# Kernel tuning notes

Hardware: AMD Instinct MI355X
Metric: run time of the kernel (lower is better)

The kernel has to match this reference:

```python
import jax, jax.numpy as jnp
import numpy as np

N = 2048          # n_nodes
H = 8             # nheads
ALPHA = 0.2       # leaky-relu slope
NEG = -9e15       # mask value used by pyGAT
# (in_dim, per-head hidden, out_dim) for the six GAT blocks of GMHAAE(256, ...)
DIMS = [(256, 128, 128), (128, 256, 256), (256, 512, 384),
        (384, 512, 256), (256, 256, 128), (128, 128, 256)]


def setup_inputs() -> dict:
    key = jax.random.key(0)
    ks = jax.random.split(key, 64)
    inp = {}
    inp["x"] = jax.random.normal(ks[0], (N, 256), dtype=jnp.float32)
    a = (jax.random.uniform(ks[1], (N, N)) < 0.01).astype(jnp.float32)
    adj = jnp.clip(jnp.maximum(a, a.T) + jnp.eye(N, dtype=jnp.float32), 0.0, 1.0)
    inp["adj"] = adj
    ki = 2
    for i, (fin, hid, fout) in enumerate(DIMS, start=1):
        s1 = (2.0 / (fin + hid)) ** 0.5
        inp[f"p{i}_Wh"] = jax.random.normal(ks[ki], (H, fin, hid), dtype=jnp.float32) * s1; ki += 1
        inp[f"p{i}_ah"] = jax.random.normal(ks[ki], (H, 2 * hid), dtype=jnp.float32) * 0.1; ki += 1
        s2 = (2.0 / (H * hid + fout)) ** 0.5
        inp[f"p{i}_Wo"] = jax.random.normal(ks[ki], (H * hid, fout), dtype=jnp.float32) * s2; ki += 1
        inp[f"p{i}_ao"] = jax.random.normal(ks[ki], (2 * fout,), dtype=jnp.float32) * 0.1; ki += 1
    return inp


def _gat_block(x, adj, Wh, ah, Wo, ao):
    """pyGAT GAT block: H concat heads (elu) -> single out head -> elu. Eval mode (no dropout)."""
    n = x.shape[0]
    D = Wh.shape[2]
    h = jnp.einsum('nf,hfd->hnd', x, Wh)                       # [H,N,D]
    s1 = jnp.einsum('hnd,hd->hn', h, ah[:, :D])                # a^T [Wh_i]
    s2 = jnp.einsum('hnd,hd->hn', h, ah[:, D:])                # a^T [Wh_j]
    e = jax.nn.leaky_relu(s1[:, :, None] + s2[:, None, :], ALPHA)   # [H,N,N]
    att = jax.nn.softmax(jnp.where(adj[None] > 0, e, NEG), axis=-1)
    hcat = jax.nn.elu(jnp.einsum('hnm,hmd->hnd', att, h))      # concat=True -> elu per head
    hcat = hcat.transpose(1, 0, 2).reshape(n, -1)              # [N, H*D]
    # output attention head (concat=False)
    D2 = Wo.shape[1]
    ho = hcat @ Wo                                             # [N,D2]
    eo = jax.nn.leaky_relu((ho @ ao[:D2])[:, None] + (ho @ ao[D2:])[None, :], ALPHA)
    ato = jax.nn.softmax(jnp.where(adj > 0, eo, NEG), axis=-1)
    return jax.nn.elu(ato @ ho)                                # F.elu in GAT.forward


def reference(x, adj,
              p1_Wh, p1_ah, p1_Wo, p1_ao,
              p2_Wh, p2_ah, p2_Wo, p2_ao,
              p3_Wh, p3_ah, p3_Wo, p3_ao,
              p4_Wh, p4_ah, p4_Wo, p4_ao,
              p5_Wh, p5_ah, p5_Wo, p5_ao,
              p6_Wh, p6_ah, p6_Wo, p6_ao):
    layers = [(p1_Wh, p1_ah, p1_Wo, p1_ao), (p2_Wh, p2_ah, p2_Wo, p2_ao),
              (p3_Wh, p3_ah, p3_Wo, p3_ao), (p4_Wh, p4_ah, p4_Wo, p4_ao),
              (p5_Wh, p5_ah, p5_Wo, p5_ao), (p6_Wh, p6_ah, p6_Wo, p6_ao)]
    h = x
    for (Wh, ah, Wo, ao) in layers:   # fixed 6-layer encoder-decoder stack
        h = _gat_block(h, adj, Wh, ah, Wo, ao)
    return h
```

## Files before the change

kernel.cpp:

```cpp
#include <hip/hip_runtime.h>
#include <hip/hip_bf16.h>
#include <math.h>

#define NN 2048
#define NH 8
#define LRALPHA 0.2f

typedef short bf16x8 __attribute__((ext_vector_type(8)));
typedef float f32x4  __attribute__((ext_vector_type(4)));

static __device__ __forceinline__ float lrelu(float x){ return x > 0.f ? x : LRALPHA * x; }
static __device__ __forceinline__ float elu(float x){ return x > 0.f ? x : expm1f(x); }

static __device__ __forceinline__ unsigned short f2bf(float v){
    unsigned u = __float_as_uint(v);
    unsigned r = (u + 0x7fffu + ((u >> 16) & 1u)) >> 16;
    return (unsigned short)r;
}
static __device__ __forceinline__ float bf2f(unsigned short b){
    return __uint_as_float(((unsigned)b) << 16);
}
static __device__ __forceinline__ float blo(unsigned u){ return __uint_as_float(u << 16); }
static __device__ __forceinline__ float bhi(unsigned u){ return __uint_as_float(u & 0xffff0000u); }

static __device__ __forceinline__ void gload16(const void* g, void* l){
    __builtin_amdgcn_global_load_lds((const __attribute__((address_space(1))) void*)g,
                                     (__attribute__((address_space(3))) void*)l, 16, 0, 0);
}

__global__ void k_count(const float* __restrict__ adj, int* __restrict__ deg) {
    int gw   = (blockIdx.x * blockDim.x + threadIdx.x) >> 6;
    int lane = threadIdx.x & 63;
    if (gw >= NN) return;
    const float* row = adj + (size_t)gw * NN;
    int cnt = 0;
    for (int j = lane; j < NN; j += 64) cnt += (row[j] > 0.f) ? 1 : 0;
    #pragma unroll
    for (int off = 32; off; off >>= 1) cnt += __shfl_down(cnt, off);
    if (lane == 0) deg[gw] = cnt;
}

__global__ void k_scan(const int* __restrict__ deg, int* __restrict__ rp) {
    __shared__ int a[NN], b[NN];
    int t = threadIdx.x;
    for (int i = t; i < NN; i += 1024) a[i] = deg[i];
    __syncthreads();
    int* src = a; int* dst = b;
    for (int off = 1; off < NN; off <<= 1) {
        for (int i = t; i < NN; i += 1024)
            dst[i] = src[i] + (i >= off ? src[i - off] : 0);
        __syncthreads();
        int* tmp = src; src = dst; dst = tmp;
    }
    for (int i = t; i < NN; i += 1024) rp[i + 1] = src[i];
    if (t == 0) rp[0] = 0;
}

__global__ void k_fill(const float* __restrict__ adj, const int* __restrict__ rp,
                       int* __restrict__ ci) {
    int gw   = (blockIdx.x * blockDim.x + threadIdx.x) >> 6;
    int lane = threadIdx.x & 63;
    if (gw >= NN) return;
    const float* row = adj + (size_t)gw * NN;
    int base = rp[gw];
    for (int j0 = 0; j0 < NN; j0 += 64) {
        bool v = row[j0 + lane] > 0.f;
        unsigned long long m = __ballot(v);
        int pos = __popcll(m & ((1ULL << lane) - 1ULL));
        if (v) ci[base + pos] = j0 + lane;
        base += __popcll(m);
    }
}

__global__ void k_split(const float* __restrict__ src, unsigned short* __restrict__ hi,
                        unsigned short* __restrict__ lo, int n4) {
    int i = blockIdx.x * 256 + threadIdx.x;
    if (i >= n4) return;
    float4 v = ((const float4*)src)[i];
    ushort4 h, l;
    h.x = f2bf(v.x); l.x = f2bf(v.x - bf2f(h.x));
    h.y = f2bf(v.y); l.y = f2bf(v.y - bf2f(h.y));
    h.z = f2bf(v.z); l.z = f2bf(v.z - bf2f(h.z));
    h.w = f2bf(v.w); l.w = f2bf(v.w - bf2f(h.w));
    ((ushort4*)hi)[i] = h;
    ((ushort4*)lo)[i] = l;
}

struct TSDesc {
    const float* B[12];
    unsigned short* bh[12];
    unsigned short* bl[12];
    int K[12], Nc[12], hs[12];
    int start[13];
};

__global__ __launch_bounds__(256) void k_tsplit_all(TSDesc d) {
    __shared__ float t[64][65];
    int b = blockIdx.x;
    int s = 0;
    while (b >= d.start[s + 1]) s++;
    int lb = b - d.start[s];
    int K = d.K[s], Nc = d.Nc[s], hs = d.hs[s];
    int tilesX = K >> 6;
    int kb = (lb % tilesX) * 64, cb = (lb / tilesX) * 64;
    const float* B = d.B[s];
    unsigned short* bth = d.bh[s];
    unsigned short* btl = d.bl[s];

    int tid = threadIdx.x;
    #pragma unroll
    for (int i = 0; i < 16; i++) {
        int idx = i * 256 + tid;
        int kk = idx >> 6, cc = idx & 63;
        int c = cb + cc, k = kb + kk;
        float v;
        if (hs < 0) v = B[(size_t)k * Nc + c];
        else {
            int hid = 1 << hs; int head = c >> hs; int dd = c & (hid - 1);
            v = B[((size_t)head * K + k) * hid + dd];
        }
        t[kk][cc] = v;
    }
    __syncthreads();
    #pragma unroll
    for (int i = 0; i < 16; i++) {
        int idx = i * 256 + tid;
        int cc = idx >> 6, kk = idx & 63;
        float v = t[kk][cc];
        unsigned short h = f2bf(v);
        size_t o = (size_t)(cb + cc) * K + kb + kk;
        bth[o] = h;
        btl[o] = f2bf(v - bf2f(h));
    }
}

template<int OUT, int NT>
__global__ __launch_bounds__(256) void k_mfma(
    const unsigned short* __restrict__ Ah, const unsigned short* __restrict__ Al,
    const unsigned short* __restrict__ Bh, const unsigned short* __restrict__ Bl,
    float* __restrict__ Cf, unsigned short* __restrict__ Cb, int Nc, int K, int Kc,
    const float* __restrict__ avec, float* __restrict__ sg1, float* __restrict__ sg2,
    int hs, int aoff, int nx, int nz, int zcol)
{
    constexpr int ALB = 4096;
    constexpr int BHB = (NT == 3) ? 8192 : 4096;
    constexpr int BLB = BHB + 2048;
    __shared__ unsigned short lds[(NT == 3) ? 12288 : 8192];
    int tid = threadIdx.x, lane = tid & 63, w = tid >> 6;

    int g = blockIdx.x;
    int xcd = g & 7, q = g >> 3;
    int x, y, z;
    if (zcol) {
        int zper = nz >> 3;
        z = xcd + 8 * (q % zper);
        int r = q / zper;
        int nxy = nx * 16;
        int r2 = r + xcd * (nxy >> 3); if (r2 >= nxy) r2 -= nxy;
        x = r2 % nx; y = r2 / nx;
    } else {
        y = xcd + 8 * (q & 1);
        x = q >> 1; z = 0;
    }
    int m0 = y * 128, n0 = x * 64;
    int kbeg = z * Kc;

    int ra0 = tid >> 2;       int ga0 = ((tid & 3) - (ra0 >> 1)) & 3;
    int ra1 = 64 + (tid >> 2); int ga1 = ((tid & 3) - (ra1 >> 1)) & 3;
    int rb  = tid >> 2;       int gb  = ((tid & 3) - (rb >> 1)) & 3;
    const unsigned short* pAh0 = Ah + (size_t)(m0 + ra0) * K + kbeg + ga0 * 8;
    const unsigned short* pAh1 = Ah + (size_t)(m0 + ra1) * K + kbeg + ga1 * 8;
    const unsigned short* pAl0 = (NT == 3) ? Al + (size_t)(m0 + ra0) * K + kbeg + ga0 * 8 : nullptr;
    const unsigned short* pAl1 = (NT == 3) ? Al + (size_t)(m0 + ra1) * K + kbeg + ga1 * 8 : nullptr;
    const unsigned short* pBh  = Bh + (size_t)(n0 + rb) * K + kbeg + gb * 8;
    const unsigned short* pBl  = Bl + (size_t)(n0 + rb) * K + kbeg + gb * 8;
    unsigned short* dA0 = &lds[w * 512];
    unsigned short* dA1 = &lds[2048 + w * 512];
    unsigned short* dB  = &lds[BHB + w * 512];

    int wr = w >> 1, wc = w & 1;
    int offA[4], offB[2];
    #pragma unroll
    for (int m = 0; m < 4; m++) {
        int row = wr * 64 + m * 16 + (lane & 15); int gg = lane >> 4;
        offA[m] = (row * 4 + ((gg + (row >> 1)) & 3)) * 8;
    }
    #pragma unroll
    for (int n = 0; n < 2; n++) {
        int row = wc * 32 + n * 16 + (lane & 15); int gg = lane >> 4;
        offB[n] = (row * 4 + ((gg + (row >> 1)) & 3)) * 8;
    }

    f32x4 acc[4][2];
    #pragma unroll
    for (int m = 0; m < 4; m++)
        #pragma unroll
        for (int n = 0; n < 2; n++) acc[m][n] = (f32x4){0.f, 0.f, 0.f, 0.f};

    int nk = Kc >> 5;
    for (int ks = 0; ks < nk; ks++) {
        gload16(pAh0, dA0);
        gload16(pAh1, dA1);
        if (NT == 3) { gload16(pAl0, dA0 + ALB); gload16(pAl1, dA1 + ALB); }
        gload16(pBh, dB);
        gload16(pBl, dB + 2048);
        pAh0 += 32; pAh1 += 32;
        if (NT == 3) { pAl0 += 32; pAl1 += 32; }
        pBh += 32; pBl += 32;
        __syncthreads();
        bf16x8 ah[4], al[4], bh[2], bl[2];
        #pragma unroll
        for (int m = 0; m < 4; m++) {
            ah[m] = *(const bf16x8*)&lds[offA[m]];
            if (NT == 3) al[m] = *(const bf16x8*)&lds[ALB + offA[m]];
        }
        #pragma unroll
        for (int n = 0; n < 2; n++) {
            bh[n] = *(const bf16x8*)&lds[BHB + offB[n]];
            bl[n] = *(const bf16x8*)&lds[BLB + offB[n]];
        }
        #pragma unroll
        for (int m = 0; m < 4; m++)
            #pragma unroll
            for (int n = 0; n < 2; n++) {
                acc[m][n] = __builtin_amdgcn_mfma_f32_16x16x32_bf16(ah[m], bh[n], acc[m][n], 0, 0, 0);
                if (NT == 3)
                    acc[m][n] = __builtin_amdgcn_mfma_f32_16x16x32_bf16(al[m], bh[n], acc[m][n], 0, 0, 0);
                acc[m][n] = __builtin_amdgcn_mfma_f32_16x16x32_bf16(ah[m], bl[n], acc[m][n], 0, 0, 0);
            }
        __syncthreads();
    }

    size_t pbase = (size_t)z * NN * Nc;
    #pragma unroll
    for (int m = 0; m < 4; m++)
        #pragma unroll
        for (int n = 0; n < 2; n++) {
            int row = m0 + wr * 64 + m * 16 + (lane >> 4) * 4;
            int col = n0 + wc * 32 + n * 16 + (lane & 15);
            #pragma unroll
            for (int r = 0; r < 4; r++) {
                float v = acc[m][n][r];
                if (OUT == 0) Cb[(size_t)(row + r) * Nc + col] = f2bf(v);
                else          Cf[pbase + (size_t)(row + r) * Nc + col] = v;
            }
        }

    if (OUT == 0) {
        int head = (hs >= 0) ? (n0 >> hs) : 0;
        const float* ab = avec + head * 2 * aoff;
        float av1[2], av2[2];
        int colbase = n0 + wc * 32 + (lane & 15);
        #pragma unroll
        for (int n = 0; n < 2; n++) {
            int c = colbase + n * 16;
            int dd = (hs >= 0) ? (c & (aoff - 1)) : c;
            av1[n] = ab[dd];
            av2[n] = ab[dd + aoff];
        }
        #pragma unroll
        for (int m = 0; m < 4; m++)
            #pragma unroll
            for (int r = 0; r < 4; r++) {
                float p1 = 0.f, p2 = 0.f;
                #pragma unroll
                for (int n = 0; n < 2; n++) {
                    float v = acc[m][n][r];
                    p1 += v * av1[n];
                    p2 += v * av2[n];
                }
                #pragma unroll
                for (int o = 1; o < 16; o <<= 1) {
                    p1 += __shfl_xor(p1, o);
                    p2 += __shfl_xor(p2, o);
                }
                if ((lane & 15) == 0) {
                    int row = m0 + wr * 64 + m * 16 + (lane >> 4) * 4 + r;
                    atomicAdd(&sg1[head * NN + row], p1);
                    atomicAdd(&sg2[head * NN + row], p2);
                }
            }
    }
}

__global__ __launch_bounds__(256) void k_red(
    const float* __restrict__ part, float* __restrict__ ho,
    const float* __restrict__ ao, float* __restrict__ t1, float* __restrict__ t2,
    int fout, int sko)
{
    int wid = threadIdx.x >> 6;
    int lane = threadIdx.x & 63;
    int row = blockIdx.x * 4 + wid;
    int C4 = fout >> 2;
    const float4* p4 = (const float4*)part;
    size_t stride4 = (size_t)NN * C4;
    float d1 = 0.f, d2 = 0.f;
    for (int c = lane; c < C4; c += 64) {
        size_t o = (size_t)row * C4 + c;
        float4 s = p4[o];
        for (int zz = 1; zz < sko; zz++) {
            float4 v = p4[o + (size_t)zz * stride4];
            s.x += v.x; s.y += v.y; s.z += v.z; s.w += v.w;
        }
        ((float4*)ho)[o] = s;
        int cc = c * 4;
        d1 += s.x * ao[cc]        + s.y * ao[cc + 1]
            + s.z * ao[cc + 2]    + s.w * ao[cc + 3];
        d2 += s.x * ao[fout + cc]     + s.y * ao[fout + cc + 1]
            + s.z * ao[fout + cc + 2] + s.w * ao[fout + cc + 3];
    }
    #pragma unroll
    for (int o = 32; o; o >>= 1) { d1 += __shfl_xor(d1, o); d2 += __shfl_xor(d2, o); }
    if (lane == 0) { t1[row] = d1; t2[row] = d2; }
}

__global__ __launch_bounds__(256) void k_aggb(
    const unsigned short* __restrict__ hh, const float* __restrict__ s1,
    const float* __restrict__ s2, const int* __restrict__ rp, const int* __restrict__ ci,
    unsigned short* __restrict__ outH, int hid, int HD, int c8sh)
{
    __shared__ float    wls[256];
    __shared__ unsigned cls[256];

    int tid = threadIdx.x;
    int wid = tid >> 6;
    int lane = tid & 63;
    int head = blockIdx.x & (NH - 1);
    int i    = (blockIdx.x >> 3) * 4 + wid;
    float* wlsw = wls + wid * 64;
    unsigned* clsw = cls + wid * 64;

    int base = rp[i], deg = rp[i + 1] - base;
    float s1i = s1[head * NN + i];
    const float* s2h = s2 + head * NN;

    int C8  = 1 << c8sh;
    int G   = 64 >> c8sh;
    int col = lane & (C8 - 1);
    int grp = lane >> c8sh;

    const uint4* h4 = (const uint4*)hh;
    unsigned hoff8 = (unsigned)(head * hid) >> 3;
    unsigned ld8   = (unsigned)HD >> 3;

    float m_run = -1e30f, s_run = 0.f;
    float a0=0,a1=0,a2=0,a3=0,a4=0,a5=0,a6=0,a7=0;

    for (int k0 = 0; k0 < deg; k0 += 64) {
        int n = min(64, deg - k0);
        float e = -1e30f;
        unsigned coff = 0;
        if (lane < n) {
            int j = ci[base + k0 + lane];
            e = lrelu(s1i + s2h[j]);
            coff = (unsigned)j * ld8 + hoff8;
        }
        float bm = e;
        #pragma unroll
        for (int o = 32; o; o >>= 1) bm = fmaxf(bm, __shfl_xor(bm, o));
        float m2 = fmaxf(m_run, bm);
        float wv = (lane < n) ? expf(e - m2) : 0.f;
        float bs = wv;
        #pragma unroll
        for (int o = 32; o; o >>= 1) bs += __shfl_xor(bs, o);
        float scale = expf(m_run - m2);
        s_run = s_run * scale + bs;
        a0*=scale; a1*=scale; a2*=scale; a3*=scale;
        a4*=scale; a5*=scale; a6*=scale; a7*=scale;
        m_run = m2;
        wlsw[lane] = wv;
        clsw[lane] = coff;

        float q0=0,q1=0,q2=0,q3=0,q4=0,q5=0,q6=0,q7=0;
        int k = grp;
        for (; k + G < n; k += 2 * G) {
            float w0 = wlsw[k], w1 = wlsw[k + G];
            uint4 u0 = h4[clsw[k]     + col];
            uint4 u1 = h4[clsw[k + G] + col];
            a0 += w0 * blo(u0.x); a1 += w0 * bhi(u0.x);
            a2 += w0 * blo(u0.y); a3 += w0 * bhi(u0.y);
            a4 += w0 * blo(u0.z); a5 += w0 * bhi(u0.z);
            a6 += w0 * blo(u0.w); a7 += w0 * bhi(u0.w);
            q0 += w1 * blo(u1.x); q1 += w1 * bhi(u1.x);
            q2 += w1 * blo(u1.y); q3 += w1 * bhi(u1.y);
            q4 += w1 * blo(u1.z); q5 += w1 * bhi(u1.z);
            q6 += w1 * blo(u1.w); q7 += w1 * bhi(u1.w);
        }
        if (k < n) {
            float w0 = wlsw[k];
            uint4 u0 = h4[clsw[k] + col];
            a0 += w0 * blo(u0.x); a1 += w0 * bhi(u0.x);
            a2 += w0 * blo(u0.y); a3 += w0 * bhi(u0.y);
            a4 += w0 * blo(u0.z); a5 += w0 * bhi(u0.z);
            a6 += w0 * blo(u0.w); a7 += w0 * bhi(u0.w);
        }
        a0+=q0; a1+=q1; a2+=q2; a3+=q3; a4+=q4; a5+=q5; a6+=q6; a7+=q7;
    }

    #pragma unroll
    for (int o = 64; o > 1; o >>= 1) {
        if (o > C8) {
            int m = o >> 1;
            a0 += __shfl_xor(a0, m); a1 += __shfl_xor(a1, m);
            a2 += __shfl_xor(a2, m); a3 += __shfl_xor(a3, m);
            a4 += __shfl_xor(a4, m); a5 += __shfl_xor(a5, m);
            a6 += __shfl_xor(a6, m); a7 += __shfl_xor(a7, m);
        }
    }

    if (grp == 0) {
        float inv = 1.f / s_run;
        float v[8] = {a0*inv,a1*inv,a2*inv,a3*inv,a4*inv,a5*inv,a6*inv,a7*inv};
        #pragma unroll
        for (int e2 = 0; e2 < 8; e2++) v[e2] = elu(v[e2]);
        unsigned short hh_[8];
        #pragma unroll
        for (int e2 = 0; e2 < 8; e2++) hh_[e2] = f2bf(v[e2]);
        size_t ob = ((size_t)i * HD + head * hid) >> 3;
        uint4 ph;
        ph.x = (unsigned)hh_[0] | ((unsigned)hh_[1] << 16);
        ph.y = (unsigned)hh_[2] | ((unsigned)hh_[3] << 16);
        ph.z = (unsigned)hh_[4] | ((unsigned)hh_[5] << 16);
        ph.w = (unsigned)hh_[6] | ((unsigned)hh_[7] << 16);
        ((uint4*)outH)[ob + col] = ph;
    }
}

__global__ __launch_bounds__(256) void k_aggs(
    const float* __restrict__ hsrc, const float* __restrict__ t1, const float* __restrict__ t2,
    const int* __restrict__ rp, const int* __restrict__ ci,
    float* __restrict__ outF, unsigned short* __restrict__ outH,
    int fout, int SCtot)
{
    __shared__ float    wls[256];
    __shared__ unsigned cls[256];

    int tid = threadIdx.x;
    int wid = tid >> 6;
    int lane = tid & 63;
    int task = blockIdx.x * 4 + wid;
    int i   = task / SCtot;
    int sc  = task - i * SCtot;
    float* wlsw = wls + wid * 64;
    unsigned* clsw = cls + wid * 64;

    int base = rp[i], deg = rp[i + 1] - base;
    float s1i = t1[i];

    int C4tot = fout >> 2;
    int soff  = sc * 64;
    int C4s   = min(64, C4tot - soff);
    int c4sh  = 31 - __clz(C4s);
    int col = lane & (C4s - 1);
    int grp = lane >> c4sh;
    int G   = 64 >> c4sh;

    const float4* h4 = (const float4*)hsrc;
    unsigned ld4 = (unsigned)fout >> 2;

    float m_run = -1e30f, s_run = 0.f;
    float4 acc = make_float4(0.f, 0.f, 0.f, 0.f);

    for (int k0 = 0; k0 < deg; k0 += 64) {
        int n = min(64, deg - k0);
        float e = -1e30f;
        unsigned coff = 0;
        if (lane < n) {
            int j = ci[base + k0 + lane];
            e = lrelu(s1i + t2[j]);
            coff = (unsigned)j * ld4 + soff;
        }
        float bm = e;
        #pragma unroll
        for (int o = 32; o; o >>= 1) bm = fmaxf(bm, __shfl_xor(bm, o));
        float m2 = fmaxf(m_run, bm);
        float wv = (lane < n) ? expf(e - m2) : 0.f;
        float bs = wv;
        #pragma unroll
        for (int o = 32; o; o >>= 1) bs += __shfl_xor(bs, o);
        float scale = expf(m_run - m2);
        s_run = s_run * scale + bs;
        acc.x *= scale; acc.y *= scale; acc.z *= scale; acc.w *= scale;
        m_run = m2;
        wlsw[lane] = wv;
        clsw[lane] = coff;

        float4 q = make_float4(0,0,0,0);
        int k = grp;
        for (; k + G < n; k += 2 * G) {
            float w0 = wlsw[k], w1 = wlsw[k + G];
            float4 h0 = h4[clsw[k]     + col];
            float4 h1 = h4[clsw[k + G] + col];
            acc.x += w0 * h0.x; acc.y += w0 * h0.y; acc.z += w0 * h0.z; acc.w += w0 * h0.w;
            q.x   += w1 * h1.x; q.y   += w1 * h1.y; q.z   += w1 * h1.z; q.w   += w1 * h1.w;
        }
        if (k < n) {
            float w0 = wlsw[k];
            float4 h0 = h4[clsw[k] + col];
            acc.x += w0 * h0.x; acc.y += w0 * h0.y; acc.z += w0 * h0.z; acc.w += w0 * h0.w;
        }
        acc.x += q.x; acc.y += q.y; acc.z += q.z; acc.w += q.w;
    }

    #pragma unroll
    for (int o = 64; o > 1; o >>= 1) {
        if (o > C4s) {
            int m = o >> 1;
            acc.x += __shfl_xor(acc.x, m); acc.y += __shfl_xor(acc.y, m);
            acc.z += __shfl_xor(acc.z, m); acc.w += __shfl_xor(acc.w, m);
        }
    }

    if (grp == 0) {
        float inv = 1.f / s_run;
        float4 val;
        val.x = elu(acc.x * inv); val.y = elu(acc.y * inv);
        val.z = elu(acc.z * inv); val.w = elu(acc.w * inv);
        size_t o4 = (size_t)i * ld4 + soff + col;
        if (outF) ((float4*)outF)[o4] = val;
        ushort4 h;
        h.x = f2bf(val.x); h.y = f2bf(val.y);
        h.z = f2bf(val.z); h.w = f2bf(val.w);
        ((ushort4*)outH)[o4] = h;
    }
}

extern "C" void kernel_launch(void* const* d_in, const int* in_sizes, int n_in,
                              void* d_out, int out_size, void* d_ws, size_t ws_size,
                              hipStream_t stream)
{
    const float* x   = (const float*)d_in[0];
    const float* adj = (const float*)d_in[1];
    struct L { int fin, hid, fout; };
    const L dims[6] = {{256,128,128},{128,256,256},{256,512,384},
                       {384,512,256},{256,256,128},{128,128,256}};
    const int SKwo[6] = {16, 8, 8, 8, 16, 8};
    const int SB = 2 * NH * NN;

    char* ws = (char*)d_ws;
    size_t off = 0;
    auto alloc = [&](size_t bytes) -> void* {
        void* p = ws + off;
        off = (off + bytes + 255) & ~(size_t)255;
        return p;
    };
    int*   rp   = (int*)alloc((NN + 1) * sizeof(int));
    int*   deg  = (int*)alloc(NN * sizeof(int));
    int*   ci   = (int*)alloc((size_t)(1 << 20) * sizeof(int));
    unsigned short* hh  = (unsigned short*)alloc((size_t)NN * 4096 * 2);
    unsigned short* ghi = (unsigned short*)alloc((size_t)NN * 4096 * 2);
    unsigned short* xhi = (unsigned short*)alloc((size_t)NN * 512 * 2);
    unsigned short* xlo = (unsigned short*)alloc((size_t)NN * 512 * 2);
    float* sball  = (float*)alloc((size_t)6 * SB * sizeof(float));
    float* hopart = (float*)alloc((size_t)NN * 3072 * sizeof(float));
    float* ho     = (float*)alloc((size_t)NN * 384 * sizeof(float));
    float* t12    = (float*)alloc((size_t)2 * NN * sizeof(float));

    unsigned short* whh[6]; unsigned short* whl[6];
    unsigned short* woh[6]; unsigned short* wol[6];
    TSDesc td;
    int nblk = 0;
    for (int l = 0; l < 6; l++) {
        int fin = dims[l].fin, hid = dims[l].hid, fout = dims[l].fout;
        int HD = NH * hid;
        size_t szWh = (size_t)fin * HD, szWo = (size_t)HD * fout;
        whh[l] = (unsigned short*)alloc(szWh * 2);
        whl[l] = (unsigned short*)alloc(szWh * 2);
        woh[l] = (unsigned short*)alloc(szWo * 2);
        wol[l] = (unsigned short*)alloc(szWo * 2);
        int hs = (hid == 128) ? 7 : (hid == 256) ? 8 : 9;
        td.B[2*l] = (const float*)d_in[2 + l * 4 + 0];
        td.bh[2*l] = whh[l]; td.bl[2*l] = whl[l];
        td.K[2*l] = fin; td.Nc[2*l] = HD; td.hs[2*l] = hs;
        td.start[2*l] = nblk; nblk += (fin / 64) * (HD / 64);
        td.B[2*l+1] = (const float*)d_in[2 + l * 4 + 2];
        td.bh[2*l+1] = woh[l]; td.bl[2*l+1] = wol[l];
        td.K[2*l+1] = HD; td.Nc[2*l+1] = fout; td.hs[2*l+1] = -1;
        td.start[2*l+1] = nblk; nblk += (HD / 64) * (fout / 64);
    }
    td.start[12] = nblk;

    hipMemsetAsync(sball, 0, (size_t)6 * SB * sizeof(float), stream);
    k_count<<<NN / 4, 256, 0, stream>>>(adj, deg);
    k_scan <<<1, 1024, 0, stream>>>(deg, rp);
    k_fill <<<NN / 4, 256, 0, stream>>>(adj, rp, ci);
    k_split<<<(NN * 256 / 4 + 255) / 256, 256, 0, stream>>>(x, xhi, xlo, NN * 256 / 4);
    k_tsplit_all<<<nblk, 256, 0, stream>>>(td);

    for (int l = 0; l < 6; l++) {
        int fin = dims[l].fin, hid = dims[l].hid, fout = dims[l].fout;
        int HD = NH * hid;
        int hs = (hid == 128) ? 7 : (hid == 256) ? 8 : 9;
        int c8sh = hs - 3;
        const float* ah = (const float*)d_in[2 + l * 4 + 1];
        const float* ao = (const float*)d_in[2 + l * 4 + 3];

        float* s1 = sball + (size_t)l * SB;
        float* s2 = s1 + NH * NN;
        float* t1 = t12;
        float* t2 = t12 + NN;

        int nx1 = HD / 64;
        if (l == 0)
            k_mfma<0,3><<<nx1 * 16, 256, 0, stream>>>(xhi, xlo, whh[l], whl[l], nullptr, hh, HD,
                                                      fin, fin, ah, s1, s2, hs, hid, nx1, 1, 0);
        else
            k_mfma<0,2><<<nx1 * 16, 256, 0, stream>>>(xhi, nullptr, whh[l], whl[l], nullptr, hh, HD,
                                                      fin, fin, ah, s1, s2, hs, hid, nx1, 1, 0);

        k_aggb<<<NN * NH / 4, 256, 0, stream>>>(hh, s1, s2, rp, ci, ghi, hid, HD, c8sh);

        int sko = SKwo[l];
        int nx2 = fout / 64;
        k_mfma<1,2><<<nx2 * 16 * sko, 256, 0, stream>>>(ghi, nullptr, woh[l], wol[l], hopart,
                                                        nullptr, fout, HD, HD / sko,
                                                        nullptr, nullptr, nullptr, -1, fout,
                                                        nx2, sko, 1);

        k_red<<<NN / 4, 256, 0, stream>>>(hopart, ho, ao, t1, t2, fout, sko);

        float* outF = (l == 5) ? (float*)d_out : nullptr;
        int SCtot = (fout / 4 + 63) / 64;
        k_aggs<<<NN * SCtot / 4, 256, 0, stream>>>(ho, t1, t2, rp, ci, outF, xhi, fout, SCtot);
    }
}
```

Measured before the change: 454.8 us.

## Precompute normalized edge softmax weights in separate kernels before aggregation

Splits each attention aggregation into two kernels. A new kernel computes normalized softmax weights per edge (per head) with a two-pass max/sum over the CSR neighbors and stores them in a workspace buffer. The aggregation kernels then just load these weights and drop the online-softmax rescaling and the final normalization. This avoids recomputing the softmax in every column-slice/head block, at the cost of extra kernel launches, an extra pass over the neighbor lists, and weight-buffer traffic. EMAX caps the edge count at 131072.

```diff
diff --git a/kernel.cpp b/kernel.cpp
--- a/kernel.cpp
+++ b/kernel.cpp
@@ -5,6 +5,7 @@
 #define NN 2048
 #define NH 8
 #define LRALPHA 0.2f
+#define EMAX (1 << 17)
 
 typedef short bf16x8 __attribute__((ext_vector_type(8)));
 typedef float f32x4  __attribute__((ext_vector_type(4)));
@@ -314,9 +315,83 @@
     if (lane == 0) { t1[row] = d1; t2[row] = d2; }
 }
 
-__global__ __launch_bounds__(256) void k_aggb(
-    const unsigned short* __restrict__ hh, const float* __restrict__ s1,
-    const float* __restrict__ s2, const int* __restrict__ rp, const int* __restrict__ ci,
+__global__ __launch_bounds__(256) void k_w(
+    const float* __restrict__ s1, const float* __restrict__ s2,
+    const int* __restrict__ rp, const int* __restrict__ ci,
+    float* __restrict__ wt)
+{
+    int wid = threadIdx.x >> 6, lane = threadIdx.x & 63;
+    int i = blockIdx.x * 4 + wid;
+    int base = rp[i], deg = rp[i + 1] - base;
+    #pragma unroll 1
+    for (int h = 0; h < NH; h++) {
+        float s1i = s1[h * NN + i];
+        const float* s2h = s2 + h * NN;
+        float m = -1e30f, s = 0.f;
+        for (int k0 = 0; k0 < deg; k0 += 64) {
+            int n = min(64, deg - k0);
+            float e = -1e30f;
+            if (lane < n) e = lrelu(s1i + s2h[ci[base + k0 + lane]]);
+            float bm = e;
+            #pragma unroll
+            for (int o = 32; o; o >>= 1) bm = fmaxf(bm, __shfl_xor(bm, o));
+            float m2 = fmaxf(m, bm);
+            float wv = (lane < n) ? expf(e - m2) : 0.f;
+            float bs = wv;
+            #pragma unroll
+            for (int o = 32; o; o >>= 1) bs += __shfl_xor(bs, o);
+            s = s * expf(m - m2) + bs;
+            m = m2;
+        }
+        float inv = 1.f / s;
+        for (int k0 = 0; k0 < deg; k0 += 64) {
+            int n = min(64, deg - k0);
+            if (lane < n) {
+                float e = lrelu(s1i + s2h[ci[base + k0 + lane]]);
+                wt[(size_t)h * EMAX + base + k0 + lane] = expf(e - m) * inv;
+            }
+        }
+    }
+}
+
+__global__ __launch_bounds__(256) void k_wo(
+    const float* __restrict__ t1, const float* __restrict__ t2,
+    const int* __restrict__ rp, const int* __restrict__ ci,
+    float* __restrict__ wto)
+{
+    int wid = threadIdx.x >> 6, lane = threadIdx.x & 63;
+    int i = blockIdx.x * 4 + wid;
+    int base = rp[i], deg = rp[i + 1] - base;
+    float s1i = t1[i];
+    float m = -1e30f, s = 0.f;
+    for (int k0 = 0; k0 < deg; k0 += 64) {
+        int n = min(64, deg - k0);
+        float e = -1e30f;
+        if (lane < n) e = lrelu(s1i + t2[ci[base + k0 + lane]]);
+        float bm = e;
+        #pragma unroll
+        for (int o = 32; o; o >>= 1) bm = fmaxf(bm, __shfl_xor(bm, o));
+        float m2 = fmaxf(m, bm);
+        float wv = (lane < n) ? expf(e - m2) : 0.f;
+        float bs = wv;
+        #pragma unroll
+        for (int o = 32; o; o >>= 1) bs += __shfl_xor(bs, o);
+        s = s * expf(m - m2) + bs;
+        m = m2;
+    }
+    float inv = 1.f / s;
+    for (int k0 = 0; k0 < deg; k0 += 64) {
+        int n = min(64, deg - k0);
+        if (lane < n) {
+            float e = lrelu(s1i + t2[ci[base + k0 + lane]]);
+            wto[base + k0 + lane] = expf(e - m) * inv;
+        }
+    }
+}
+
+__global__ __launch_bounds__(256) void k_gab(
+    const unsigned short* __restrict__ hh, const float* __restrict__ wt,
+    const int* __restrict__ rp, const int* __restrict__ ci,
     unsigned short* __restrict__ outH, int hid, int HD, int c8sh)
 {
     __shared__ float    wls[256];
@@ -331,8 +406,7 @@
     unsigned* clsw = cls + wid * 64;
 
     int base = rp[i], deg = rp[i + 1] - base;
-    float s1i = s1[head * NN + i];
-    const float* s2h = s2 + head * NN;
+    const float* wth = wt + (size_t)head * EMAX + base;
 
     int C8  = 1 << c8sh;
     int G   = 64 >> c8sh;
@@ -343,34 +417,14 @@
     unsigned hoff8 = (unsigned)(head * hid) >> 3;
     unsigned ld8   = (unsigned)HD >> 3;
 
-    float m_run = -1e30f, s_run = 0.f;
     float a0=0,a1=0,a2=0,a3=0,a4=0,a5=0,a6=0,a7=0;
 
     for (int k0 = 0; k0 < deg; k0 += 64) {
         int n = min(64, deg - k0);
-        float e = -1e30f;
-        unsigned coff = 0;
         if (lane < n) {
-            int j = ci[base + k0 + lane];
-            e = lrelu(s1i + s2h[j]);
-            coff = (unsigned)j * ld8 + hoff8;
-        }
-        float bm = e;
-        #pragma unroll
-        for (int o = 32; o; o >>= 1) bm = fmaxf(bm, __shfl_xor(bm, o));
-        float m2 = fmaxf(m_run, bm);
-        float wv = (lane < n) ? expf(e - m2) : 0.f;
-        float bs = wv;
-        #pragma unroll
-        for (int o = 32; o; o >>= 1) bs += __shfl_xor(bs, o);
-        float scale = expf(m_run - m2);
-        s_run = s_run * scale + bs;
-        a0*=scale; a1*=scale; a2*=scale; a3*=scale;
-        a4*=scale; a5*=scale; a6*=scale; a7*=scale;
-        m_run = m2;
-        wlsw[lane] = wv;
-        clsw[lane] = coff;
-
+            wlsw[lane] = wth[k0 + lane];
+            clsw[lane] = (unsigned)ci[base + k0 + lane] * ld8 + hoff8;
+        }
         float q0=0,q1=0,q2=0,q3=0,q4=0,q5=0,q6=0,q7=0;
         int k = grp;
         for (; k + G < n; k += 2 * G) {
@@ -409,8 +463,7 @@
     }
 
     if (grp == 0) {
-        float inv = 1.f / s_run;
-        float v[8] = {a0*inv,a1*inv,a2*inv,a3*inv,a4*inv,a5*inv,a6*inv,a7*inv};
+        float v[8] = {a0,a1,a2,a3,a4,a5,a6,a7};
         #pragma unroll
         for (int e2 = 0; e2 < 8; e2++) v[e2] = elu(v[e2]);
         unsigned short hh_[8];
@@ -426,8 +479,8 @@
     }
 }
 
-__global__ __launch_bounds__(256) void k_aggs(
-    const float* __restrict__ hsrc, const float* __restrict__ t1, const float* __restrict__ t2,
+__global__ __launch_bounds__(256) void k_gas(
+    const float* __restrict__ hsrc, const float* __restrict__ wto,
     const int* __restrict__ rp, const int* __restrict__ ci,
     float* __restrict__ outF, unsigned short* __restrict__ outH,
     int fout, int SCtot)
@@ -445,7 +498,6 @@
     unsigned* clsw = cls + wid * 64;
 
     int base = rp[i], deg = rp[i + 1] - base;
-    float s1i = t1[i];
 
     int C4tot = fout >> 2;
     int soff  = sc * 64;
@@ -458,33 +510,14 @@
     const float4* h4 = (const float4*)hsrc;
     unsigned ld4 = (unsigned)fout >> 2;
 
-    float m_run = -1e30f, s_run = 0.f;
     float4 acc = make_float4(0.f, 0.f, 0.f, 0.f);
 
     for (int k0 = 0; k0 < deg; k0 += 64) {
         int n = min(64, deg - k0);
-        float e = -1e30f;
-        unsigned coff = 0;
         if (lane < n) {
-            int j = ci[base + k0 + lane];
-            e = lrelu(s1i + t2[j]);
-            coff = (unsigned)j * ld4 + soff;
-        }
-        float bm = e;
-        #pragma unroll
-        for (int o = 32; o; o >>= 1) bm = fmaxf(bm, __shfl_xor(bm, o));
-        float m2 = fmaxf(m_run, bm);
-        float wv = (lane < n) ? expf(e - m2) : 0.f;
-        float bs = wv;
-        #pragma unroll
-        for (int o = 32; o; o >>= 1) bs += __shfl_xor(bs, o);
-        float scale = expf(m_run - m2);
-        s_run = s_run * scale + bs;
-        acc.x *= scale; acc.y *= scale; acc.z *= scale; acc.w *= scale;
-        m_run = m2;
-        wlsw[lane] = wv;
-        clsw[lane] = coff;
-
+            wlsw[lane] = wto[base + k0 + lane];
+            clsw[lane] = (unsigned)ci[base + k0 + lane] * ld4 + soff;
+        }
         float4 q = make_float4(0,0,0,0);
         int k = grp;
         for (; k + G < n; k += 2 * G) {
@@ -512,10 +545,9 @@
     }
 
     if (grp == 0) {
-        float inv = 1.f / s_run;
         float4 val;
-        val.x = elu(acc.x * inv); val.y = elu(acc.y * inv);
-        val.z = elu(acc.z * inv); val.w = elu(acc.w * inv);
+        val.x = elu(acc.x); val.y = elu(acc.y);
+        val.z = elu(acc.z); val.w = elu(acc.w);
         size_t o4 = (size_t)i * ld4 + soff + col;
         if (outF) ((float4*)outF)[o4] = val;
         ushort4 h;
@@ -555,6 +587,8 @@
     float* hopart = (float*)alloc((size_t)NN * 3072 * sizeof(float));
     float* ho     = (float*)alloc((size_t)NN * 384 * sizeof(float));
     float* t12    = (float*)alloc((size_t)2 * NN * sizeof(float));
+    float* wt     = (float*)alloc((size_t)NH * EMAX * sizeof(float));
+    float* wto    = (float*)alloc((size_t)EMAX * sizeof(float));
 
     unsigned short* whh[6]; unsigned short* whl[6];
     unsigned short* woh[6]; unsigned short* wol[6];
@@ -608,7 +642,8 @@
             k_mfma<0,2><<<nx1 * 16, 256, 0, stream>>>(xhi, nullptr, whh[l], whl[l], nullptr, hh, HD,
                                                       fin, fin, ah, s1, s2, hs, hid, nx1, 1, 0);
 
-        k_aggb<<<NN * NH / 4, 256, 0, stream>>>(hh, s1, s2, rp, ci, ghi, hid, HD, c8sh);
+        k_w<<<NN / 4, 256, 0, stream>>>(s1, s2, rp, ci, wt);
+        k_gab<<<NN * NH / 4, 256, 0, stream>>>(hh, wt, rp, ci, ghi, hid, HD, c8sh);
 
         int sko = SKwo[l];
         int nx2 = fout / 64;
@@ -619,8 +654,9 @@
 
         k_red<<<NN / 4, 256, 0, stream>>>(hopart, ho, ao, t1, t2, fout, sko);
 
+        k_wo<<<NN / 4, 256, 0, stream>>>(t1, t2, rp, ci, wto);
         float* outF = (l == 5) ? (float*)d_out : nullptr;
         int SCtot = (fout / 4 + 63) / 64;
-        k_aggs<<<NN * SCtot / 4, 256, 0, stream>>>(ho, t1, t2, rp, ci, outF, xhi, fout, SCtot);
-    }
-}
+        k_gas<<<NN * SCtot / 4, 256, 0, stream>>>(ho, wto, rp, ci, outF, xhi, fout, SCtot);
+    }
+}
```

New measurement: 561.7 us. +23.5%, slower.

## Store split-K output partials and ho in bf16, rework output aggregation

Applied to the files above, without the earlier changes.

The split-K output GEMM now writes bf16 partials instead of fp32. The reduction kernel sums these into a bf16 ho buffer, and the output-head aggregation gathers 8 bf16 values per lane with one wave per node instead of column-sliced float4 tasks. Split-K is also fixed at 8 for all layers. This halves the bytes moved for the partials and ho gathers, at the cost of extra rounding error from bf16 partial sums and bf16 ho, and idle lanes when fout is 384.

```diff
diff --git a/kernel.cpp b/kernel.cpp
--- a/kernel.cpp
+++ b/kernel.cpp
@@ -27,6 +27,12 @@
     __builtin_amdgcn_global_load_lds((const __attribute__((address_space(1))) void*)g,
                                      (__attribute__((address_space(3))) void*)l, 16, 0, 0);
 }
+
+#define ACC8(A, wv, u) \
+    A[0] += wv * blo(u.x); A[1] += wv * bhi(u.x); \
+    A[2] += wv * blo(u.y); A[3] += wv * bhi(u.y); \
+    A[4] += wv * blo(u.z); A[5] += wv * bhi(u.z); \
+    A[6] += wv * blo(u.w); A[7] += wv * bhi(u.w);
 
 __global__ void k_count(const float* __restrict__ adj, int* __restrict__ deg) {
     int gw   = (blockIdx.x * blockDim.x + threadIdx.x) >> 6;
@@ -138,7 +144,7 @@
 __global__ __launch_bounds__(256) void k_mfma(
     const unsigned short* __restrict__ Ah, const unsigned short* __restrict__ Al,
     const unsigned short* __restrict__ Bh, const unsigned short* __restrict__ Bl,
-    float* __restrict__ Cf, unsigned short* __restrict__ Cb, int Nc, int K, int Kc,
+    unsigned short* __restrict__ Cb, int Nc, int K, int Kc,
     const float* __restrict__ avec, float* __restrict__ sg1, float* __restrict__ sg2,
     int hs, int aoff, int nx, int nz, int zcol)
 {
@@ -239,11 +245,8 @@
             int row = m0 + wr * 64 + m * 16 + (lane >> 4) * 4;
             int col = n0 + wc * 32 + n * 16 + (lane & 15);
             #pragma unroll
-            for (int r = 0; r < 4; r++) {
-                float v = acc[m][n][r];
-                if (OUT == 0) Cb[(size_t)(row + r) * Nc + col] = f2bf(v);
-                else          Cf[pbase + (size_t)(row + r) * Nc + col] = v;
-            }
+            for (int r = 0; r < 4; r++)
+                Cb[pbase + (size_t)(row + r) * Nc + col] = f2bf(acc[m][n][r]);
         }
 
     if (OUT == 0) {
@@ -284,30 +287,41 @@
 }
 
 __global__ __launch_bounds__(256) void k_red(
-    const float* __restrict__ part, float* __restrict__ ho,
+    const unsigned short* __restrict__ part, unsigned short* __restrict__ ho,
     const float* __restrict__ ao, float* __restrict__ t1, float* __restrict__ t2,
     int fout, int sko)
 {
     int wid = threadIdx.x >> 6;
     int lane = threadIdx.x & 63;
     int row = blockIdx.x * 4 + wid;
-    int C4 = fout >> 2;
-    const float4* p4 = (const float4*)part;
-    size_t stride4 = (size_t)NN * C4;
+    int C8 = fout >> 3;
+    const uint4* p8 = (const uint4*)part;
+    size_t stride8 = (size_t)NN * C8;
     float d1 = 0.f, d2 = 0.f;
-    for (int c = lane; c < C4; c += 64) {
-        size_t o = (size_t)row * C4 + c;
-        float4 s = p4[o];
-        for (int zz = 1; zz < sko; zz++) {
-            float4 v = p4[o + (size_t)zz * stride4];
-            s.x += v.x; s.y += v.y; s.z += v.z; s.w += v.w;
-        }
-        ((float4*)ho)[o] = s;
-        int cc = c * 4;
-        d1 += s.x * ao[cc]        + s.y * ao[cc + 1]
-            + s.z * ao[cc + 2]    + s.w * ao[cc + 3];
-        d2 += s.x * ao[fout + cc]     + s.y * ao[fout + cc + 1]
-            + s.z * ao[fout + cc + 2] + s.w * ao[fout + cc + 3];
+    if (lane < C8) {
+        size_t o = (size_t)row * C8 + lane;
+        float s[8];
+        #pragma unroll
+        for (int e = 0; e < 8; e++) s[e] = 0.f;
+        for (int zz = 0; zz < sko; zz++) {
+            uint4 u = p8[o + (size_t)zz * stride8];
+            ACC8(s, 1.f, u);
+        }
+        unsigned short hb[8];
+        #pragma unroll
+        for (int e = 0; e < 8; e++) hb[e] = f2bf(s[e]);
+        uint4 ph;
+        ph.x = (unsigned)hb[0] | ((unsigned)hb[1] << 16);
+        ph.y = (unsigned)hb[2] | ((unsigned)hb[3] << 16);
+        ph.z = (unsigned)hb[4] | ((unsigned)hb[5] << 16);
+        ph.w = (unsigned)hb[6] | ((unsigned)hb[7] << 16);
+        ((uint4*)ho)[o] = ph;
+        int cc = lane * 8;
+        #pragma unroll
+        for (int e = 0; e < 8; e++) {
+            d1 += s[e] * ao[cc + e];
+            d2 += s[e] * ao[fout + cc + e];
+        }
     }
     #pragma unroll
     for (int o = 32; o; o >>= 1) { d1 += __shfl_xor(d1, o); d2 += __shfl_xor(d2, o); }
@@ -344,7 +358,9 @@
     unsigned ld8   = (unsigned)HD >> 3;
 
     float m_run = -1e30f, s_run = 0.f;
-    float a0=0,a1=0,a2=0,a3=0,a4=0,a5=0,a6=0,a7=0;
+    float aA[8], qB[8];
+    #pragma unroll
+    for (int e = 0; e < 8; e++) { aA[e] = 0.f; qB[e] = 0.f; }
 
     for (int k0 = 0; k0 < deg; k0 += 64) {
         int n = min(64, deg - k0);
@@ -365,72 +381,56 @@
         for (int o = 32; o; o >>= 1) bs += __shfl_xor(bs, o);
         float scale = expf(m_run - m2);
         s_run = s_run * scale + bs;
-        a0*=scale; a1*=scale; a2*=scale; a3*=scale;
-        a4*=scale; a5*=scale; a6*=scale; a7*=scale;
+        #pragma unroll
+        for (int e2 = 0; e2 < 8; e2++) aA[e2] *= scale;
         m_run = m2;
         wlsw[lane] = wv;
         clsw[lane] = coff;
 
-        float q0=0,q1=0,q2=0,q3=0,q4=0,q5=0,q6=0,q7=0;
         int k = grp;
         for (; k + G < n; k += 2 * G) {
             float w0 = wlsw[k], w1 = wlsw[k + G];
             uint4 u0 = h4[clsw[k]     + col];
             uint4 u1 = h4[clsw[k + G] + col];
-            a0 += w0 * blo(u0.x); a1 += w0 * bhi(u0.x);
-            a2 += w0 * blo(u0.y); a3 += w0 * bhi(u0.y);
-            a4 += w0 * blo(u0.z); a5 += w0 * bhi(u0.z);
-            a6 += w0 * blo(u0.w); a7 += w0 * bhi(u0.w);
-            q0 += w1 * blo(u1.x); q1 += w1 * bhi(u1.x);
-            q2 += w1 * blo(u1.y); q3 += w1 * bhi(u1.y);
-            q4 += w1 * blo(u1.z); q5 += w1 * bhi(u1.z);
-            q6 += w1 * blo(u1.w); q7 += w1 * bhi(u1.w);
+            ACC8(aA, w0, u0);
+            ACC8(qB, w1, u1);
         }
         if (k < n) {
             float w0 = wlsw[k];
             uint4 u0 = h4[clsw[k] + col];
-            a0 += w0 * blo(u0.x); a1 += w0 * bhi(u0.x);
-            a2 += w0 * blo(u0.y); a3 += w0 * bhi(u0.y);
-            a4 += w0 * blo(u0.z); a5 += w0 * bhi(u0.z);
-            a6 += w0 * blo(u0.w); a7 += w0 * bhi(u0.w);
-        }
-        a0+=q0; a1+=q1; a2+=q2; a3+=q3; a4+=q4; a5+=q5; a6+=q6; a7+=q7;
-    }
-
-    #pragma unroll
-    for (int o = 64; o > 1; o >>= 1) {
-        if (o > C8) {
-            int m = o >> 1;
-            a0 += __shfl_xor(a0, m); a1 += __shfl_xor(a1, m);
-            a2 += __shfl_xor(a2, m); a3 += __shfl_xor(a3, m);
-            a4 += __shfl_xor(a4, m); a5 += __shfl_xor(a5, m);
-            a6 += __shfl_xor(a6, m); a7 += __shfl_xor(a7, m);
+            ACC8(aA, w0, u0);
+        }
+    }
+    #pragma unroll
+    for (int e2 = 0; e2 < 8; e2++) aA[e2] += qB[e2];
+
+    #pragma unroll
+    for (int m = 32; m >= 1; m >>= 1) {
+        if (m >= C8) {
+            #pragma unroll
+            for (int e2 = 0; e2 < 8; e2++) aA[e2] += __shfl_xor(aA[e2], m);
         }
     }
 
     if (grp == 0) {
         float inv = 1.f / s_run;
-        float v[8] = {a0*inv,a1*inv,a2*inv,a3*inv,a4*inv,a5*inv,a6*inv,a7*inv};
-        #pragma unroll
-        for (int e2 = 0; e2 < 8; e2++) v[e2] = elu(v[e2]);
-        unsigned short hh_[8];
-        #pragma unroll
-        for (int e2 = 0; e2 < 8; e2++) hh_[e2] = f2bf(v[e2]);
+        unsigned short hb[8];
+        #pragma unroll
+        for (int e2 = 0; e2 < 8; e2++) hb[e2] = f2bf(elu(aA[e2] * inv));
         size_t ob = ((size_t)i * HD + head * hid) >> 3;
         uint4 ph;
-        ph.x = (unsigned)hh_[0] | ((unsigned)hh_[1] << 16);
-        ph.y = (unsigned)hh_[2] | ((unsigned)hh_[3] << 16);
-        ph.z = (unsigned)hh_[4] | ((unsigned)hh_[5] << 16);
-        ph.w = (unsigned)hh_[6] | ((unsigned)hh_[7] << 16);
+        ph.x = (unsigned)hb[0] | ((unsigned)hb[1] << 16);
+        ph.y = (unsigned)hb[2] | ((unsigned)hb[3] << 16);
+        ph.z = (unsigned)hb[4] | ((unsigned)hb[5] << 16);
+        ph.w = (unsigned)hb[6] | ((unsigned)hb[7] << 16);
         ((uint4*)outH)[ob + col] = ph;
     }
 }
 
 __global__ __launch_bounds__(256) void k_aggs(
-    const float* __restrict__ hsrc, const float* __restrict__ t1, const float* __restrict__ t2,
-    const int* __restrict__ rp, const int* __restrict__ ci,
-    float* __restrict__ outF, unsigned short* __restrict__ outH,
-    int fout, int SCtot)
+    const unsigned short* __restrict__ ho, const float* __restrict__ t1,
+    const float* __restrict__ t2, const int* __restrict__ rp, const int* __restrict__ ci,
+    float* __restrict__ outF, unsigned short* __restrict__ outH, int fout)
 {
     __shared__ float    wls[256];
     __shared__ unsigned cls[256];
@@ -438,28 +438,28 @@
     int tid = threadIdx.x;
     int wid = tid >> 6;
     int lane = tid & 63;
-    int task = blockIdx.x * 4 + wid;
-    int i   = task / SCtot;
-    int sc  = task - i * SCtot;
+    int i = blockIdx.x * 4 + wid;
     float* wlsw = wls + wid * 64;
     unsigned* clsw = cls + wid * 64;
 
     int base = rp[i], deg = rp[i + 1] - base;
     float s1i = t1[i];
 
-    int C4tot = fout >> 2;
-    int soff  = sc * 64;
-    int C4s   = min(64, C4tot - soff);
-    int c4sh  = 31 - __clz(C4s);
-    int col = lane & (C4s - 1);
-    int grp = lane >> c4sh;
-    int G   = 64 >> c4sh;
-
-    const float4* h4 = (const float4*)hsrc;
-    unsigned ld4 = (unsigned)fout >> 2;
+    int C8s = fout >> 3;
+    int G, col, grp; bool act;
+    if (C8s == 48) { G = 1; col = lane; grp = 0; act = lane < 48; }
+    else {
+        int sh = 31 - __clz(C8s);
+        G = 64 >> sh; col = lane & (C8s - 1); grp = lane >> sh; act = true;
+    }
+
+    const uint4* h4 = (const uint4*)ho;
+    unsigned ld8 = (unsigned)fout >> 3;
 
     float m_run = -1e30f, s_run = 0.f;
-    float4 acc = make_float4(0.f, 0.f, 0.f, 0.f);
+    float aA[8], qB[8];
+    #pragma unroll
+    for (int e = 0; e < 8; e++) { aA[e] = 0.f; qB[e] = 0.f; }
 
     for (int k0 = 0; k0 < deg; k0 += 64) {
         int n = min(64, deg - k0);
@@ -468,7 +468,7 @@
         if (lane < n) {
             int j = ci[base + k0 + lane];
             e = lrelu(s1i + t2[j]);
-            coff = (unsigned)j * ld4 + soff;
+            coff = (unsigned)j * ld8;
         }
         float bm = e;
         #pragma unroll
@@ -480,48 +480,59 @@
         for (int o = 32; o; o >>= 1) bs += __shfl_xor(bs, o);
         float scale = expf(m_run - m2);
         s_run = s_run * scale + bs;
-        acc.x *= scale; acc.y *= scale; acc.z *= scale; acc.w *= scale;
+        #pragma unroll
+        for (int e2 = 0; e2 < 8; e2++) aA[e2] *= scale;
         m_run = m2;
         wlsw[lane] = wv;
         clsw[lane] = coff;
 
-        float4 q = make_float4(0,0,0,0);
-        int k = grp;
-        for (; k + G < n; k += 2 * G) {
-            float w0 = wlsw[k], w1 = wlsw[k + G];
-            float4 h0 = h4[clsw[k]     + col];
-            float4 h1 = h4[clsw[k + G] + col];
-            acc.x += w0 * h0.x; acc.y += w0 * h0.y; acc.z += w0 * h0.z; acc.w += w0 * h0.w;
-            q.x   += w1 * h1.x; q.y   += w1 * h1.y; q.z   += w1 * h1.z; q.w   += w1 * h1.w;
-        }
-        if (k < n) {
-            float w0 = wlsw[k];
-            float4 h0 = h4[clsw[k] + col];
-            acc.x += w0 * h0.x; acc.y += w0 * h0.y; acc.z += w0 * h0.z; acc.w += w0 * h0.w;
-        }
-        acc.x += q.x; acc.y += q.y; acc.z += q.z; acc.w += q.w;
-    }
-
-    #pragma unroll
-    for (int o = 64; o > 1; o >>= 1) {
-        if (o > C4s) {
-            int m = o >> 1;
-            acc.x += __shfl_xor(acc.x, m); acc.y += __shfl_xor(acc.y, m);
-            acc.z += __shfl_xor(acc.z, m); acc.w += __shfl_xor(acc.w, m);
-        }
-    }
-
-    if (grp == 0) {
+        if (act) {
+            int k = grp;
+            for (; k + G < n; k += 2 * G) {
+                float w0 = wlsw[k], w1 = wlsw[k + G];
+                uint4 u0 = h4[clsw[k]     + col];
+                uint4 u1 = h4[clsw[k + G] + col];
+                ACC8(aA, w0, u0);
+                ACC8(qB, w1, u1);
+            }
+            if (k < n) {
+                float w0 = wlsw[k];
+                uint4 u0 = h4[clsw[k] + col];
+                ACC8(aA, w0, u0);
+            }
+        }
+    }
+    #pragma unroll
+    for (int e2 = 0; e2 < 8; e2++) aA[e2] += qB[e2];
+
+    #pragma unroll
+    for (int m = 32; m >= 1; m >>= 1) {
+        if (m >= C8s) {
+            #pragma unroll
+            for (int e2 = 0; e2 < 8; e2++) aA[e2] += __shfl_xor(aA[e2], m);
+        }
+    }
+
+    if (grp == 0 && act) {
         float inv = 1.f / s_run;
-        float4 val;
-        val.x = elu(acc.x * inv); val.y = elu(acc.y * inv);
-        val.z = elu(acc.z * inv); val.w = elu(acc.w * inv);
-        size_t o4 = (size_t)i * ld4 + soff + col;
-        if (outF) ((float4*)outF)[o4] = val;
-        ushort4 h;
-        h.x = f2bf(val.x); h.y = f2bf(val.y);
-        h.z = f2bf(val.z); h.w = f2bf(val.w);
-        ((ushort4*)outH)[o4] = h;
+        float v[8];
+        #pragma unroll
+        for (int e2 = 0; e2 < 8; e2++) v[e2] = elu(aA[e2] * inv);
+        size_t ob = (size_t)i * C8s + col;
+        if (outF) {
+            size_t o4 = ob * 2;
+            ((float4*)outF)[o4]     = make_float4(v[0], v[1], v[2], v[3]);
+            ((float4*)outF)[o4 + 1] = make_float4(v[4], v[5], v[6], v[7]);
+        }
+        unsigned short hb[8];
+        #pragma unroll
+        for (int e2 = 0; e2 < 8; e2++) hb[e2] = f2bf(v[e2]);
+        uint4 ph;
+        ph.x = (unsigned)hb[0] | ((unsigned)hb[1] << 16);
+        ph.y = (unsigned)hb[2] | ((unsigned)hb[3] << 16);
+        ph.z = (unsigned)hb[4] | ((unsigned)hb[5] << 16);
+        ph.w = (unsigned)hb[6] | ((unsigned)hb[7] << 16);
+        ((uint4*)outH)[ob] = ph;
     }
 }
 
@@ -534,7 +545,7 @@
     struct L { int fin, hid, fout; };
     const L dims[6] = {{256,128,128},{128,256,256},{256,512,384},
                        {384,512,256},{256,256,128},{128,128,256}};
-    const int SKwo[6] = {16, 8, 8, 8, 16, 8};
+    const int SKO = 8;
     const int SB = 2 * NH * NN;
 
     char* ws = (char*)d_ws;
@@ -552,8 +563,8 @@
     unsigned short* xhi = (unsigned short*)alloc((size_t)NN * 512 * 2);
     unsigned short* xlo = (unsigned short*)alloc((size_t)NN * 512 * 2);
     float* sball  = (float*)alloc((size_t)6 * SB * sizeof(float));
-    float* hopart = (float*)alloc((size_t)NN * 3072 * sizeof(float));
-    float* ho     = (float*)alloc((size_t)NN * 384 * sizeof(float));
+    unsigned short* hopart = (unsigned short*)alloc((size_t)NN * 3072 * 2);
+    unsigned short* ho     = (unsigned short*)alloc((size_t)NN * 384 * 2);
     float* t12    = (float*)alloc((size_t)2 * NN * sizeof(float));
 
     unsigned short* whh[6]; unsigned short* whl[6];
@@ -602,25 +613,23 @@
 
         int nx1 = HD / 64;
         if (l == 0)
-            k_mfma<0,3><<<nx1 * 16, 256, 0, stream>>>(xhi, xlo, whh[l], whl[l], nullptr, hh, HD,
+            k_mfma<0,3><<<nx1 * 16, 256, 0, stream>>>(xhi, xlo, whh[l], whl[l], hh, HD,
                                                       fin, fin, ah, s1, s2, hs, hid, nx1, 1, 0);
         else
-            k_mfma<0,2><<<nx1 * 16, 256, 0, stream>>>(xhi, nullptr, whh[l], whl[l], nullptr, hh, HD,
+            k_mfma<0,2><<<nx1 * 16, 256, 0, stream>>>(xhi, nullptr, whh[l], whl[l], hh, HD,
                                                       fin, fin, ah, s1, s2, hs, hid, nx1, 1, 0);
 
         k_aggb<<<NN * NH / 4, 256, 0, stream>>>(hh, s1, s2, rp, ci, ghi, hid, HD, c8sh);
 
-        int sko = SKwo[l];
         int nx2 = fout / 64;
-        k_mfma<1,2><<<nx2 * 16 * sko, 256, 0, stream>>>(ghi, nullptr, woh[l], wol[l], hopart,
-                                                        nullptr, fout, HD, HD / sko,
+        k_mfma<1,2><<<nx2 * 16 * SKO, 256, 0, stream>>>(ghi, nullptr, woh[l], wol[l], hopart,
+                                                        fout, HD, HD / SKO,
                                                         nullptr, nullptr, nullptr, -1, fout,
-                                                        nx2, sko, 1);
-
-        k_red<<<NN / 4, 256, 0, stream>>>(hopart, ho, ao, t1, t2, fout, sko);
+                                                        nx2, SKO, 1);
+
+        k_red<<<NN / 4, 256, 0, stream>>>(hopart, ho, ao, t1, t2, fout, SKO);
 
         float* outF = (l == 5) ? (float*)d_out : nullptr;
-        int SCtot = (fout / 4 + 63) / 64;
-        k_aggs<<<NN * SCtot / 4, 256, 0, stream>>>(ho, t1, t2, rp, ci, outF, xhi, fout, SCtot);
-    }
-}
+        k_aggs<<<NN / 4, 256, 0, stream>>>(ho, t1, t2, rp, ci, outF, xhi, fout);
+    }
+}
```

Result: faster. 433.3 us (-4.7%).
